# Optimization experiments

Hardware: AMD Instinct MI355X
Metric: run time of the kernel (lower is better)

Reference implementation:

```python
import jax, jax.numpy as jnp
import numpy as np

ALPHA = 10.0   # args.alpha softmax sharpness
EPS = 1e-8     # torch CosineSimilarity eps


def setup_inputs() -> dict:
    key = jax.random.key(0)
    k0, k1, k2, k3 = jax.random.split(key, 4)
    B, S, F, D, C = 8, 1024, 32, 128, 16
    Hs = jax.random.normal(k0, (B, S, F, D), dtype=jnp.float32)
    Cj = jax.random.normal(k1, (C, D), dtype=jnp.float32)
    W = jax.random.normal(k2, (D, D), dtype=jnp.float32) * 0.05  # nn.Linear weight [out,in]
    b = jnp.zeros((D,), dtype=jnp.float32)
    importance = jax.random.uniform(k3, (B, S, F), dtype=jnp.float32)
    return {"Hs": Hs, "Cj": Cj, "W": W, "b": b, "importance": importance}


def reference(Hs, Cj, W, b, importance):
    # Hs: [B,S,F,D] features; Cj: [C,D] cluster centers; importance: [B,S,F]
    # Faithful to Model_DTSSOCC.assignment (importance is not None branch),
    # but avoids materializing the broadcasted [B,S,F,C,D] repeat tensors.
    Hn = Hs / jnp.maximum(jnp.linalg.norm(Hs, axis=-1, keepdims=True), EPS)
    Cn = Cj / jnp.maximum(jnp.linalg.norm(Cj, axis=-1, keepdims=True), EPS)
    cos = jnp.einsum('bsfd,cd->bsfc', Hn, Cn)            # cosine_sim4 over dim D
    logits = -ALPHA * 0.5 * (1.0 - cos)                  # -alpha * dists, [B,S,F,C]
    w3 = jax.nn.softmax(logits, axis=3)                  # softmax over centers
    w = jax.nn.softmax(logits, axis=2)                   # softmax over feas
    w3 = jnp.swapaxes(w3, 2, 3)                          # [B,S,C,F]
    w = jnp.swapaxes(w, 2, 3)                            # [B,S,C,F]
    F_tj = jax.nn.relu(jnp.einsum('bsfd,ed->bsfe', Hs, W) + b)  # relu(Linear(F_t))
    # importance update: bmm(w3, importance) then softmax over centers
    imp = jax.nn.softmax(jnp.einsum('bscf,bsf->bsc', w3, importance), axis=2)
    # weighted feature aggregation: bmm(w, F_tj) -> [B,S,C,D]
    f_t_new = jnp.einsum('bscf,bsfd->bscd', w, F_tj)
    return f_t_new, imp
```

## Files before the change

### kernel.cpp

```cpp
#include <hip/hip_runtime.h>
#include <hip/hip_bf16.h>
#include <math.h>

constexpr int Bn = 8, Sn = 1024, Fn = 32, Dn = 128, Cc = 16;
constexpr int NSITE = Bn * Sn;

#define EPSV 1e-8f

typedef __attribute__((ext_vector_type(8))) short bf16x8;
typedef __attribute__((ext_vector_type(4))) short bf16x4;
typedef __attribute__((ext_vector_type(4))) float f32x4;

__device__ inline short f2bf(float x) {
    __hip_bfloat16 h = __float2bfloat16(x);
    short s;
    __builtin_memcpy(&s, &h, sizeof(s));
    return s;
}

__device__ inline bf16x8 cvt8(float4 x0, float4 x1) {
    bf16x8 r;
    r[0] = f2bf(x0.x); r[1] = f2bf(x0.y); r[2] = f2bf(x0.z); r[3] = f2bf(x0.w);
    r[4] = f2bf(x1.x); r[5] = f2bf(x1.y); r[6] = f2bf(x1.z); r[7] = f2bf(x1.w);
    return r;
}

__device__ inline float dot4(float4 v) {
    return v.x * v.x + v.y * v.y + v.z * v.z + v.w * v.w;
}

__global__ void normC_kernel(const float* __restrict__ Cj, short* __restrict__ CnPack) {
    int c = blockIdx.x;
    int d = threadIdx.x;
    float v = Cj[c * Dn + d];
    float sq = v * v;
    #pragma unroll
    for (int off = 32; off > 0; off >>= 1) sq += __shfl_down(sq, off);
    __shared__ float part[2];
    if ((d & 63) == 0) part[d >> 6] = sq;
    __syncthreads();
    float nrm = sqrtf(part[0] + part[1]);
    float cn = v / fmaxf(nrm, EPSV);
    int kt = d >> 5, ln = ((d >> 3) & 3) * 16 + c, j = d & 7;
    CnPack[(kt * 64 + ln) * 8 + j] = f2bf(cn);
}

__global__ void packW_kernel(const float* __restrict__ W, short* __restrict__ Wb) {
    int t = blockIdx.x * 256 + threadIdx.x;
    int n = t >> 7, k = t & 127;
    short v = f2bf(W[n * Dn + k]);
    int frag = (n >> 4) * 4 + (k >> 5);
    int lane = ((k >> 3) & 3) * 16 + (n & 15);
    int j = k & 7;
    Wb[(frag * 64 + lane) * 8 + j] = v;
}

__launch_bounds__(64, 4)
__global__ void site_kernel(const float* __restrict__ Hs,
                            const short* __restrict__ CnPack,
                            const short* __restrict__ Wb,
                            const float* __restrict__ bvec,
                            const float* __restrict__ imp_in,
                            float* __restrict__ f_out,
                            float* __restrict__ imp_out) {
    __shared__ __align__(16) short F_tjT[128][40];
    __shared__ __align__(16) short sWgT[16][40];

    const int lane = threadIdx.x;
    const int c16  = lane & 15;
    const int g    = lane >> 4;
    const int site = blockIdx.x;

    const float* hsrc = Hs + (size_t)site * (Fn * Dn);
    const f32x4 zro = {0.f, 0.f, 0.f, 0.f};

    bf16x8 bcf[4];
    #pragma unroll
    for (int kt = 0; kt < 4; ++kt)
        bcf[kt] = *(const bf16x8*)&CnPack[(kt * 64 + lane) * 8];

    float impv[2][4];
    #pragma unroll
    for (int mt = 0; mt < 2; ++mt)
        #pragma unroll
        for (int r = 0; r < 4; ++r)
            impv[mt][r] = imp_in[(size_t)site * Fn + 16 * mt + 4 * g + r];

    bf16x8 aF[2][4];
    float sq0 = 0.f, sq1 = 0.f;
    #pragma unroll
    for (int kt = 0; kt < 4; ++kt) {
        const float* p0 = hsrc + c16 * Dn + kt * 32 + g * 8;
        const float* p1 = hsrc + (16 + c16) * Dn + kt * 32 + g * 8;
        float4 a0 = *(const float4*)p0, a1 = *(const float4*)(p0 + 4);
        float4 b0 = *(const float4*)p1, b1 = *(const float4*)(p1 + 4);
        sq0 += dot4(a0) + dot4(a1);
        sq1 += dot4(b0) + dot4(b1);
        aF[0][kt] = cvt8(a0, a1);
        aF[1][kt] = cvt8(b0, b1);
    }
    sq0 += __shfl_xor(sq0, 16); sq0 += __shfl_xor(sq0, 32);
    sq1 += __shfl_xor(sq1, 16); sq1 += __shfl_xor(sq1, 32);
    float inv0 = 1.0f / fmaxf(sqrtf(sq0), EPSV);
    float inv1 = 1.0f / fmaxf(sqrtf(sq1), EPSV);

    f32x4 cos0 = zro, cos1 = zro;
    #pragma unroll
    for (int kt = 0; kt < 4; ++kt) {
        cos0 = __builtin_amdgcn_mfma_f32_16x16x32_bf16(aF[0][kt], bcf[kt], cos0, 0, 0, 0);
        cos1 = __builtin_amdgcn_mfma_f32_16x16x32_bf16(aF[1][kt], bcf[kt], cos1, 0, 0, 0);
    }

    #pragma unroll
    for (int nt = 0; nt < 8; ++nt) {
        bf16x8 bw0 = *(const bf16x8*)&Wb[((nt * 4) + 0) * 512 + lane * 8];
        bf16x8 bw1 = *(const bf16x8*)&Wb[((nt * 4) + 1) * 512 + lane * 8];
        bf16x8 bw2 = *(const bf16x8*)&Wb[((nt * 4) + 2) * 512 + lane * 8];
        bf16x8 bw3 = *(const bf16x8*)&Wb[((nt * 4) + 3) * 512 + lane * 8];
        f32x4 acc0 = zro, acc1 = zro;
        acc0 = __builtin_amdgcn_mfma_f32_16x16x32_bf16(aF[0][0], bw0, acc0, 0, 0, 0);
        acc1 = __builtin_amdgcn_mfma_f32_16x16x32_bf16(aF[1][0], bw0, acc1, 0, 0, 0);
        acc0 = __builtin_amdgcn_mfma_f32_16x16x32_bf16(aF[0][1], bw1, acc0, 0, 0, 0);
        acc1 = __builtin_amdgcn_mfma_f32_16x16x32_bf16(aF[1][1], bw1, acc1, 0, 0, 0);
        acc0 = __builtin_amdgcn_mfma_f32_16x16x32_bf16(aF[0][2], bw2, acc0, 0, 0, 0);
        acc1 = __builtin_amdgcn_mfma_f32_16x16x32_bf16(aF[1][2], bw2, acc1, 0, 0, 0);
        acc0 = __builtin_amdgcn_mfma_f32_16x16x32_bf16(aF[0][3], bw3, acc0, 0, 0, 0);
        acc1 = __builtin_amdgcn_mfma_f32_16x16x32_bf16(aF[1][3], bw3, acc1, 0, 0, 0);
        float bb = bvec[nt * 16 + c16];
        bf16x4 p0, p1;
        #pragma unroll
        for (int r = 0; r < 4; ++r) {
            p0[r] = f2bf(fmaxf(acc0[r] + bb, 0.f));
            p1[r] = f2bf(fmaxf(acc1[r] + bb, 0.f));
        }
        *(bf16x4*)&F_tjT[nt * 16 + c16][4 * g]      = p0;
        *(bf16x4*)&F_tjT[nt * 16 + c16][16 + 4 * g] = p1;
    }

    float s0[4], s1[4];
    #pragma unroll
    for (int r = 0; r < 4; ++r) {
        s0[r] = 5.0f * cos0[r] * __shfl(inv0, 4 * g + r);
        s1[r] = 5.0f * cos1[r] * __shfl(inv1, 4 * g + r);
    }
    {
        float m = s0[0];
        #pragma unroll
        for (int r = 0; r < 4; ++r) { m = fmaxf(m, s0[r]); m = fmaxf(m, s1[r]); }
        m = fmaxf(m, __shfl_xor(m, 16));
        m = fmaxf(m, __shfl_xor(m, 32));
        float e0[4], e1[4], sum = 0.f;
        #pragma unroll
        for (int r = 0; r < 4; ++r) {
            e0[r] = __expf(s0[r] - m); e1[r] = __expf(s1[r] - m);
            sum += e0[r] + e1[r];
        }
        sum += __shfl_xor(sum, 16);
        sum += __shfl_xor(sum, 32);
        float inv = 1.0f / sum;
        #pragma unroll
        for (int r = 0; r < 4; ++r) {
            sWgT[c16][4 * g + r]      = f2bf(e0[r] * inv);
            sWgT[c16][16 + 4 * g + r] = f2bf(e1[r] * inv);
        }
    }
    {
        float t = 0.f;
        #pragma unroll
        for (int h = 0; h < 2; ++h) {
            #pragma unroll
            for (int r = 0; r < 4; ++r) {
                float sv = h ? s1[r] : s0[r];
                float m3 = sv;
                m3 = fmaxf(m3, __shfl_xor(m3, 1));
                m3 = fmaxf(m3, __shfl_xor(m3, 2));
                m3 = fmaxf(m3, __shfl_xor(m3, 4));
                m3 = fmaxf(m3, __shfl_xor(m3, 8));
                float e3 = __expf(sv - m3);
                float q3 = e3;
                q3 += __shfl_xor(q3, 1);
                q3 += __shfl_xor(q3, 2);
                q3 += __shfl_xor(q3, 4);
                q3 += __shfl_xor(q3, 8);
                t += (e3 / q3) * impv[h][r];
            }
        }
        t += __shfl_xor(t, 16);
        t += __shfl_xor(t, 32);
        float mi = t;
        mi = fmaxf(mi, __shfl_xor(mi, 1));
        mi = fmaxf(mi, __shfl_xor(mi, 2));
        mi = fmaxf(mi, __shfl_xor(mi, 4));
        mi = fmaxf(mi, __shfl_xor(mi, 8));
        float ei = __expf(t - mi);
        float si = ei;
        si += __shfl_xor(si, 1);
        si += __shfl_xor(si, 2);
        si += __shfl_xor(si, 4);
        si += __shfl_xor(si, 8);
        if (g == 0) imp_out[(size_t)site * Cc + c16] = ei / si;
    }

    {
        bf16x8 wA = *(const bf16x8*)&sWgT[c16][8 * g];
        float* op = f_out + (size_t)site * (Cc * Dn);
        #pragma unroll
        for (int nt = 0; nt < 8; ++nt) {
            bf16x8 bF = *(const bf16x8*)&F_tjT[nt * 16 + c16][8 * g];
            f32x4 o = __builtin_amdgcn_mfma_f32_16x16x32_bf16(wA, bF, zro, 0, 0, 0);
            #pragma unroll
            for (int r = 0; r < 4; ++r)
                op[(4 * g + r) * Dn + nt * 16 + c16] = o[r];
        }
    }
}

extern "C" void kernel_launch(void* const* d_in, const int* in_sizes, int n_in,
                              void* d_out, int out_size, void* d_ws, size_t ws_size,
                              hipStream_t stream) {
    const float* Hs  = (const float*)d_in[0];
    const float* Cj  = (const float*)d_in[1];
    const float* W   = (const float*)d_in[2];
    const float* b   = (const float*)d_in[3];
    const float* imp = (const float*)d_in[4];

    float* f_out   = (float*)d_out;
    float* imp_out = f_out + (size_t)NSITE * Cc * Dn;

    short* CnPack = (short*)d_ws;
    short* Wb     = CnPack + Cc * Dn;

    hipLaunchKernelGGL(normC_kernel, dim3(Cc), dim3(Dn), 0, stream, Cj, CnPack);
    hipLaunchKernelGGL(packW_kernel, dim3((Dn * Dn) / 256), dim3(256), 0, stream, W, Wb);
    hipLaunchKernelGGL(site_kernel, dim3(NSITE), dim3(64), 0, stream,
                       Hs, CnPack, Wb, b, imp, f_out, imp_out);
}
```

Before: 51.08 us.

## Fuse prep kernels, use Gram MFMA for norms, vectorize output stores

Merges the two preprocessing kernels into one launch. In the site kernel, Hs is loaded with nontemporal vector loads, and row norms are taken from the diagonal of a Gram MFMA instead of scalar dot products. The softmax weights are shuffled straight into an MFMA operand, which removes the shared-memory staging buffer. The final MFMA is transposed so each lane writes contiguous f32x4 nontemporal stores. The risks are norms computed in bf16 precision and extra MFMA and shuffle work.

```diff
diff --git a/kernel.cpp b/kernel.cpp
--- a/kernel.cpp
+++ b/kernel.cpp
@@ -18,41 +18,43 @@
     return s;
 }
 
-__device__ inline bf16x8 cvt8(float4 x0, float4 x1) {
+__device__ inline bf16x8 cvt8(f32x4 x0, f32x4 x1) {
     bf16x8 r;
-    r[0] = f2bf(x0.x); r[1] = f2bf(x0.y); r[2] = f2bf(x0.z); r[3] = f2bf(x0.w);
-    r[4] = f2bf(x1.x); r[5] = f2bf(x1.y); r[6] = f2bf(x1.z); r[7] = f2bf(x1.w);
+    r[0] = f2bf(x0[0]); r[1] = f2bf(x0[1]); r[2] = f2bf(x0[2]); r[3] = f2bf(x0[3]);
+    r[4] = f2bf(x1[0]); r[5] = f2bf(x1[1]); r[6] = f2bf(x1[2]); r[7] = f2bf(x1[3]);
     return r;
 }
 
-__device__ inline float dot4(float4 v) {
-    return v.x * v.x + v.y * v.y + v.z * v.z + v.w * v.w;
-}
-
-__global__ void normC_kernel(const float* __restrict__ Cj, short* __restrict__ CnPack) {
-    int c = blockIdx.x;
-    int d = threadIdx.x;
-    float v = Cj[c * Dn + d];
-    float sq = v * v;
-    #pragma unroll
-    for (int off = 32; off > 0; off >>= 1) sq += __shfl_down(sq, off);
-    __shared__ float part[2];
-    if ((d & 63) == 0) part[d >> 6] = sq;
-    __syncthreads();
-    float nrm = sqrtf(part[0] + part[1]);
-    float cn = v / fmaxf(nrm, EPSV);
-    int kt = d >> 5, ln = ((d >> 3) & 3) * 16 + c, j = d & 7;
-    CnPack[(kt * 64 + ln) * 8 + j] = f2bf(cn);
-}
-
-__global__ void packW_kernel(const float* __restrict__ W, short* __restrict__ Wb) {
-    int t = blockIdx.x * 256 + threadIdx.x;
-    int n = t >> 7, k = t & 127;
-    short v = f2bf(W[n * Dn + k]);
-    int frag = (n >> 4) * 4 + (k >> 5);
-    int lane = ((k >> 3) & 3) * 16 + (n & 15);
-    int j = k & 7;
-    Wb[(frag * 64 + lane) * 8 + j] = v;
+__global__ void prep_kernel(const float* __restrict__ Cj,
+                            const float* __restrict__ W,
+                            short* __restrict__ CnPack,
+                            short* __restrict__ Wb) {
+    const int tid = threadIdx.x;
+    if (blockIdx.x < 64) {
+        int t = blockIdx.x * 256 + tid;
+        int n = t >> 7, k = t & 127;
+        short v = f2bf(W[n * Dn + k]);
+        int frag = (n >> 4) * 4 + (k >> 5);
+        int lane = ((k >> 3) & 3) * 16 + (n & 15);
+        Wb[(frag * 64 + lane) * 8 + (k & 7)] = v;
+    } else {
+        int c = blockIdx.x - 64;
+        __shared__ float part[2];
+        float v = 0.f, sq = 0.f;
+        if (tid < 128) {
+            v = Cj[c * Dn + tid];
+            sq = v * v;
+            #pragma unroll
+            for (int off = 32; off > 0; off >>= 1) sq += __shfl_down(sq, off);
+        }
+        if (tid < 128 && (tid & 63) == 0) part[tid >> 6] = sq;
+        __syncthreads();
+        if (tid < 128) {
+            float cn = v / fmaxf(sqrtf(part[0] + part[1]), EPSV);
+            int kt = tid >> 5, ln = ((tid >> 3) & 3) * 16 + c, j = tid & 7;
+            CnPack[(kt * 64 + ln) * 8 + j] = f2bf(cn);
+        }
+    }
 }
 
 __launch_bounds__(64, 4)
@@ -64,7 +66,6 @@
                             float* __restrict__ f_out,
                             float* __restrict__ imp_out) {
     __shared__ __align__(16) short F_tjT[128][40];
-    __shared__ __align__(16) short sWgT[16][40];
 
     const int lane = threadIdx.x;
     const int c16  = lane & 15;
@@ -74,41 +75,118 @@
     const float* hsrc = Hs + (size_t)site * (Fn * Dn);
     const f32x4 zro = {0.f, 0.f, 0.f, 0.f};
 
+    f32x4 x[16];
+    #pragma unroll
+    for (int kt = 0; kt < 4; ++kt) {
+        const f32x4* p0 = (const f32x4*)(hsrc + c16 * Dn + kt * 32 + g * 8);
+        const f32x4* p1 = (const f32x4*)(hsrc + (16 + c16) * Dn + kt * 32 + g * 8);
+        x[4 * kt + 0] = __builtin_nontemporal_load(p0);
+        x[4 * kt + 1] = __builtin_nontemporal_load(p0 + 1);
+        x[4 * kt + 2] = __builtin_nontemporal_load(p1);
+        x[4 * kt + 3] = __builtin_nontemporal_load(p1 + 1);
+    }
     bf16x8 bcf[4];
     #pragma unroll
     for (int kt = 0; kt < 4; ++kt)
         bcf[kt] = *(const bf16x8*)&CnPack[(kt * 64 + lane) * 8];
-
-    float impv[2][4];
-    #pragma unroll
-    for (int mt = 0; mt < 2; ++mt)
-        #pragma unroll
-        for (int r = 0; r < 4; ++r)
-            impv[mt][r] = imp_in[(size_t)site * Fn + 16 * mt + 4 * g + r];
+    const float* impp = imp_in + (size_t)site * Fn;
+    f32x4 impv0 = *(const f32x4*)(impp + 4 * g);
+    f32x4 impv1 = *(const f32x4*)(impp + 16 + 4 * g);
 
     bf16x8 aF[2][4];
-    float sq0 = 0.f, sq1 = 0.f;
     #pragma unroll
     for (int kt = 0; kt < 4; ++kt) {
-        const float* p0 = hsrc + c16 * Dn + kt * 32 + g * 8;
-        const float* p1 = hsrc + (16 + c16) * Dn + kt * 32 + g * 8;
-        float4 a0 = *(const float4*)p0, a1 = *(const float4*)(p0 + 4);
-        float4 b0 = *(const float4*)p1, b1 = *(const float4*)(p1 + 4);
-        sq0 += dot4(a0) + dot4(a1);
-        sq1 += dot4(b0) + dot4(b1);
-        aF[0][kt] = cvt8(a0, a1);
-        aF[1][kt] = cvt8(b0, b1);
-    }
-    sq0 += __shfl_xor(sq0, 16); sq0 += __shfl_xor(sq0, 32);
-    sq1 += __shfl_xor(sq1, 16); sq1 += __shfl_xor(sq1, 32);
-    float inv0 = 1.0f / fmaxf(sqrtf(sq0), EPSV);
-    float inv1 = 1.0f / fmaxf(sqrtf(sq1), EPSV);
-
-    f32x4 cos0 = zro, cos1 = zro;
+        aF[0][kt] = cvt8(x[4 * kt + 0], x[4 * kt + 1]);
+        aF[1][kt] = cvt8(x[4 * kt + 2], x[4 * kt + 3]);
+    }
+
+    f32x4 gm0 = zro, gm1 = zro, cos0 = zro, cos1 = zro;
     #pragma unroll
     for (int kt = 0; kt < 4; ++kt) {
+        gm0  = __builtin_amdgcn_mfma_f32_16x16x32_bf16(aF[0][kt], aF[0][kt], gm0, 0, 0, 0);
+        gm1  = __builtin_amdgcn_mfma_f32_16x16x32_bf16(aF[1][kt], aF[1][kt], gm1, 0, 0, 0);
         cos0 = __builtin_amdgcn_mfma_f32_16x16x32_bf16(aF[0][kt], bcf[kt], cos0, 0, 0, 0);
         cos1 = __builtin_amdgcn_mfma_f32_16x16x32_bf16(aF[1][kt], bcf[kt], cos1, 0, 0, 0);
+    }
+
+    float s0[4], s1[4];
+    #pragma unroll
+    for (int r = 0; r < 4; ++r) {
+        float q0 = __shfl(gm0[r], 20 * g + r);
+        float q1 = __shfl(gm1[r], 20 * g + r);
+        float i0 = 1.0f / fmaxf(sqrtf(q0), EPSV);
+        float i1 = 1.0f / fmaxf(sqrtf(q1), EPSV);
+        s0[r] = 5.0f * cos0[r] * i0;
+        s1[r] = 5.0f * cos1[r] * i1;
+    }
+
+    bf16x8 wB;
+    {
+        float m = s0[0];
+        #pragma unroll
+        for (int r = 0; r < 4; ++r) { m = fmaxf(m, s0[r]); m = fmaxf(m, s1[r]); }
+        m = fmaxf(m, __shfl_xor(m, 16));
+        m = fmaxf(m, __shfl_xor(m, 32));
+        float e0[4], e1[4], sum = 0.f;
+        #pragma unroll
+        for (int r = 0; r < 4; ++r) {
+            e0[r] = __expf(s0[r] - m); e1[r] = __expf(s1[r] - m);
+            sum += e0[r] + e1[r];
+        }
+        sum += __shfl_xor(sum, 16);
+        sum += __shfl_xor(sum, 32);
+        float inv = 1.0f / sum;
+        #pragma unroll
+        for (int r = 0; r < 4; ++r) { e0[r] *= inv; e1[r] *= inv; }
+        const int srcA = c16 + 16 * ((2 * g) & 3);
+        const int srcB = c16 + 16 * ((2 * g + 1) & 3);
+        const bool hi = (g >= 2);
+        #pragma unroll
+        for (int r = 0; r < 4; ++r) {
+            float a0 = __shfl(e0[r], srcA);
+            float a1 = __shfl(e1[r], srcA);
+            wB[r] = f2bf(hi ? a1 : a0);
+            float b0 = __shfl(e0[r], srcB);
+            float b1 = __shfl(e1[r], srcB);
+            wB[4 + r] = f2bf(hi ? b1 : b0);
+        }
+    }
+
+    {
+        float t = 0.f;
+        #pragma unroll
+        for (int h = 0; h < 2; ++h) {
+            #pragma unroll
+            for (int r = 0; r < 4; ++r) {
+                float sv = h ? s1[r] : s0[r];
+                float m3 = sv;
+                m3 = fmaxf(m3, __shfl_xor(m3, 1));
+                m3 = fmaxf(m3, __shfl_xor(m3, 2));
+                m3 = fmaxf(m3, __shfl_xor(m3, 4));
+                m3 = fmaxf(m3, __shfl_xor(m3, 8));
+                float e3 = __expf(sv - m3);
+                float q3 = e3;
+                q3 += __shfl_xor(q3, 1);
+                q3 += __shfl_xor(q3, 2);
+                q3 += __shfl_xor(q3, 4);
+                q3 += __shfl_xor(q3, 8);
+                t += (e3 / q3) * (h ? impv1[r] : impv0[r]);
+            }
+        }
+        t += __shfl_xor(t, 16);
+        t += __shfl_xor(t, 32);
+        float mi = t;
+        mi = fmaxf(mi, __shfl_xor(mi, 1));
+        mi = fmaxf(mi, __shfl_xor(mi, 2));
+        mi = fmaxf(mi, __shfl_xor(mi, 4));
+        mi = fmaxf(mi, __shfl_xor(mi, 8));
+        float ei = __expf(t - mi);
+        float si = ei;
+        si += __shfl_xor(si, 1);
+        si += __shfl_xor(si, 2);
+        si += __shfl_xor(si, 4);
+        si += __shfl_xor(si, 8);
+        if (g == 0) imp_out[(size_t)site * Cc + c16] = ei / si;
     }
 
     #pragma unroll
@@ -137,80 +215,13 @@
         *(bf16x4*)&F_tjT[nt * 16 + c16][16 + 4 * g] = p1;
     }
 
-    float s0[4], s1[4];
-    #pragma unroll
-    for (int r = 0; r < 4; ++r) {
-        s0[r] = 5.0f * cos0[r] * __shfl(inv0, 4 * g + r);
-        s1[r] = 5.0f * cos1[r] * __shfl(inv1, 4 * g + r);
-    }
     {
-        float m = s0[0];
-        #pragma unroll
-        for (int r = 0; r < 4; ++r) { m = fmaxf(m, s0[r]); m = fmaxf(m, s1[r]); }
-        m = fmaxf(m, __shfl_xor(m, 16));
-        m = fmaxf(m, __shfl_xor(m, 32));
-        float e0[4], e1[4], sum = 0.f;
-        #pragma unroll
-        for (int r = 0; r < 4; ++r) {
-            e0[r] = __expf(s0[r] - m); e1[r] = __expf(s1[r] - m);
-            sum += e0[r] + e1[r];
-        }
-        sum += __shfl_xor(sum, 16);
-        sum += __shfl_xor(sum, 32);
-        float inv = 1.0f / sum;
-        #pragma unroll
-        for (int r = 0; r < 4; ++r) {
-            sWgT[c16][4 * g + r]      = f2bf(e0[r] * inv);
-            sWgT[c16][16 + 4 * g + r] = f2bf(e1[r] * inv);
-        }
-    }
-    {
-        float t = 0.f;
-        #pragma unroll
-        for (int h = 0; h < 2; ++h) {
-            #pragma unroll
-            for (int r = 0; r < 4; ++r) {
-                float sv = h ? s1[r] : s0[r];
-                float m3 = sv;
-                m3 = fmaxf(m3, __shfl_xor(m3, 1));
-                m3 = fmaxf(m3, __shfl_xor(m3, 2));
-                m3 = fmaxf(m3, __shfl_xor(m3, 4));
-                m3 = fmaxf(m3, __shfl_xor(m3, 8));
-                float e3 = __expf(sv - m3);
-                float q3 = e3;
-                q3 += __shfl_xor(q3, 1);
-                q3 += __shfl_xor(q3, 2);
-                q3 += __shfl_xor(q3, 4);
-                q3 += __shfl_xor(q3, 8);
-                t += (e3 / q3) * impv[h][r];
-            }
-        }
-        t += __shfl_xor(t, 16);
-        t += __shfl_xor(t, 32);
-        float mi = t;
-        mi = fmaxf(mi, __shfl_xor(mi, 1));
-        mi = fmaxf(mi, __shfl_xor(mi, 2));
-        mi = fmaxf(mi, __shfl_xor(mi, 4));
-        mi = fmaxf(mi, __shfl_xor(mi, 8));
-        float ei = __expf(t - mi);
-        float si = ei;
-        si += __shfl_xor(si, 1);
-        si += __shfl_xor(si, 2);
-        si += __shfl_xor(si, 4);
-        si += __shfl_xor(si, 8);
-        if (g == 0) imp_out[(size_t)site * Cc + c16] = ei / si;
-    }
-
-    {
-        bf16x8 wA = *(const bf16x8*)&sWgT[c16][8 * g];
         float* op = f_out + (size_t)site * (Cc * Dn);
         #pragma unroll
         for (int nt = 0; nt < 8; ++nt) {
-            bf16x8 bF = *(const bf16x8*)&F_tjT[nt * 16 + c16][8 * g];
-            f32x4 o = __builtin_amdgcn_mfma_f32_16x16x32_bf16(wA, bF, zro, 0, 0, 0);
-            #pragma unroll
-            for (int r = 0; r < 4; ++r)
-                op[(4 * g + r) * Dn + nt * 16 + c16] = o[r];
+            bf16x8 aFt = *(const bf16x8*)&F_tjT[nt * 16 + c16][8 * g];
+            f32x4 o = __builtin_amdgcn_mfma_f32_16x16x32_bf16(aFt, wB, zro, 0, 0, 0);
+            __builtin_nontemporal_store(o, (f32x4*)(op + c16 * Dn + nt * 16 + 4 * g));
         }
     }
 }
@@ -230,8 +241,7 @@
     short* CnPack = (short*)d_ws;
     short* Wb     = CnPack + Cc * Dn;
 
-    hipLaunchKernelGGL(normC_kernel, dim3(Cc), dim3(Dn), 0, stream, Cj, CnPack);
-    hipLaunchKernelGGL(packW_kernel, dim3((Dn * Dn) / 256), dim3(256), 0, stream, W, Wb);
+    hipLaunchKernelGGL(prep_kernel, dim3(80), dim3(256), 0, stream, Cj, W, CnPack, Wb);
     hipLaunchKernelGGL(site_kernel, dim3(NSITE), dim3(64), 0, stream,
                        Hs, CnPack, Wb, b, imp, f_out, imp_out);
 }
```

Result: slower. 62.86 us (+23.1%).
